# Kernel optimization log

Hardware: AMD Instinct MI355X
Metric: run time of the kernel (lower is better)

## Reference

```python
import jax, jax.numpy as jnp
import numpy as np


def bilinear_resize(x, out_h, out_w):
    # x: [B, C, H, W]; matches torch F.interpolate(mode='bilinear', align_corners=False)
    B, C, H, W = x.shape
    ry = jnp.clip((jnp.arange(out_h, dtype=jnp.float32) + 0.5) * (H / out_h) - 0.5, 0.0, H - 1)
    rx = jnp.clip((jnp.arange(out_w, dtype=jnp.float32) + 0.5) * (W / out_w) - 0.5, 0.0, W - 1)
    y0 = jnp.floor(ry).astype(jnp.int32); y1 = jnp.minimum(y0 + 1, H - 1)
    x0 = jnp.floor(rx).astype(jnp.int32); x1 = jnp.minimum(x0 + 1, W - 1)
    wy = (ry - y0)[:, None]  # [out_h,1]
    wx = (rx - x0)[None, :]  # [1,out_w]
    r0 = x[:, :, y0, :]; r1 = x[:, :, y1, :]
    v00 = r0[:, :, :, x0]; v01 = r0[:, :, :, x1]
    v10 = r1[:, :, :, x0]; v11 = r1[:, :, :, x1]
    return (v00 * (1 - wx) + v01 * wx) * (1 - wy) + (v10 * (1 - wx) + v11 * wx) * wy


def setup_inputs() -> dict:
    key0 = jax.random.key(0)
    ks = jax.random.split(key0, 16)
    B, N, C, H = 2, 300, 256, 8
    hw_lvl = np.array([[64, 64], [32, 32], [16, 16]], dtype=np.int64)
    L = int((hw_lvl[:, 0] * hw_lvl[:, 1]).sum())  # 5376
    p = lambda k, sh: (0.02 * jax.random.normal(k, sh, dtype=jnp.float32))
    return {
        'query': jax.random.normal(ks[0], (B, N, C), dtype=jnp.float32),
        'key': jax.random.normal(ks[1], (B, L, C), dtype=jnp.float32),
        'value': jax.random.normal(ks[2], (B, L, C), dtype=jnp.float32),
        'key_padding_mask': jnp.zeros((B, L), dtype=bool),
        'hw_lvl': hw_lvl,
        'Wq': p(ks[3], (C, C)), 'Wk': p(ks[4], (C, C)), 'Wv': p(ks[5], (C, C)),
        'Wp': p(ks[6], (C, C)), 'bp': jnp.zeros((C,), jnp.float32),
        'W1': p(ks[7], (H, H)), 'b1': jnp.zeros((H,), jnp.float32),
        'W2': p(ks[8], (H, H)), 'b2': jnp.zeros((H,), jnp.float32),
        'W3': p(ks[9], (H, H)), 'b3': jnp.zeros((H,), jnp.float32),
        'Wm': p(ks[10], (3 * H, 1)), 'bm': jnp.zeros((1,), jnp.float32),
    }


def reference(query, key, value, key_padding_mask, hw_lvl,
              Wq, Wk, Wv, Wp, bp, W1, b1, W2, b2, W3, b3, Wm, bm):
    hw = np.asarray(hw_lvl)
    h1, wd1 = int(hw[0, 0]), int(hw[0, 1])
    h2, wd2 = int(hw[1, 0]), int(hw[1, 1])
    h3, wd3 = int(hw[2, 0]), int(hw[2, 1])
    w1 = h1 * wd1
    w2 = w1 + h2 * wd2
    B, N, C = query.shape
    L = key.shape[1]
    H = W1.shape[0]
    scale = (C // H) ** -0.5

    q = (query @ Wq).reshape(B, N, H, C // H)
    k = (key @ Wk).reshape(B, L, H, C // H)
    v = (value @ Wv).reshape(B, L, H, C // H)
    attn = jnp.einsum('bnhd,blhd->bhnl', q, k) * scale  # [B,H,N,L]

    ap = attn.transpose(0, 2, 3, 1)  # [B,N,L,H]
    f1 = jax.nn.relu(ap[:, :, :w1] @ W1 + b1)                      # [B,N,w1,H]
    f2 = jax.nn.relu(ap[:, :, w1:w2] @ W2 + b2)                    # [B,N,h2*wd2,H]
    f3 = jax.nn.relu(ap[:, :, w2:] @ W3 + b3)                      # [B,N,h3*wd3,H]
    f2 = f2.transpose(0, 1, 3, 2).reshape(B * N, H, h2, wd2)
    f3 = f3.transpose(0, 1, 3, 2).reshape(B * N, H, h3, wd3)
    f2 = bilinear_resize(f2, h1, wd1).transpose(0, 2, 3, 1).reshape(B, N, w1, H)
    f3 = bilinear_resize(f3, h1, wd1).transpose(0, 2, 3, 1).reshape(B, N, w1, H)
    new_feats = jnp.concatenate([f1, f2, f3], axis=-1)             # [B,N,w1,3H]
    mask = jax.nn.relu(new_feats @ Wm + bm)                        # [B,N,w1,1]

    aw = jax.nn.softmax(attn, axis=-1)                             # [B,H,N,L]
    x = jnp.einsum('bhnl,blhd->bnhd', aw, v).reshape(B, N, C)
    x = x @ Wp + bp
    return x, mask
```

## Files before the change

kernel.cpp:

```cpp
#include <hip/hip_runtime.h>
#include <hip/hip_bf16.h>

typedef __hip_bfloat16 bf16;
typedef __attribute__((ext_vector_type(8))) short short8v;
typedef __attribute__((ext_vector_type(8))) unsigned short ushort8v;
typedef __attribute__((ext_vector_type(4))) unsigned short ushort4v;
typedef __attribute__((ext_vector_type(4))) float float4v;

__device__ __forceinline__ float bfu2f(unsigned short u) {
    union { unsigned int i; float f; } v; v.i = ((unsigned int)u) << 16; return v.f;
}
__device__ __forceinline__ unsigned short f2bfu_rn(float x) {
    union { float f; unsigned int i; } u; u.f = x;
    unsigned int r = (u.i + 0x7FFFu + ((u.i >> 16) & 1u)) >> 16;
    return (unsigned short)r;
}

__global__ __launch_bounds__(256) void cast_wt(
    const float* __restrict__ Wq, const float* __restrict__ Wk,
    const float* __restrict__ Wv, const float* __restrict__ Wp,
    unsigned short* __restrict__ wt)
{
    __shared__ unsigned short tile[64][72];
    const float* W = (blockIdx.z == 0) ? Wq : (blockIdx.z == 1) ? Wk
                   : (blockIdx.z == 2) ? Wv : Wp;
    unsigned short* WT = wt + (size_t)blockIdx.z * 65536;
    const int t = threadIdx.x;
    const int k0 = blockIdx.x * 64, n0 = blockIdx.y * 64;
    {
        const int r = t >> 2, cseg = (t & 3) * 16;
        const float* src = W + (size_t)(k0 + r) * 256 + n0 + cseg;
        #pragma unroll
        for (int j = 0; j < 16; ++j) tile[r][cseg + j] = f2bfu_rn(src[j]);
    }
    __syncthreads();
    {
        const int ch = t & 63, lq = t >> 6;
        ushort8v o0, o1;
        #pragma unroll
        for (int i = 0; i < 8; ++i) o0[i] = tile[lq * 16 + i][ch];
        #pragma unroll
        for (int i = 0; i < 8; ++i) o1[i] = tile[lq * 16 + 8 + i][ch];
        unsigned short* dst = WT + (size_t)(n0 + ch) * 256 + k0 + lq * 16;
        *(ushort8v*)(dst)     = o0;
        *(ushort8v*)(dst + 8) = o1;
    }
}

__device__ __forceinline__ void proj_core(
    const float* __restrict__ aptr, const unsigned short* __restrict__ Wt,
    int nc0, int m16, int quad, float4v acc[8])
{
    #pragma unroll
    for (int i = 0; i < 8; ++i) acc[i] = (float4v){0.f, 0.f, 0.f, 0.f};
    #pragma unroll
    for (int ks = 0; ks < 8; ++ks) {
        float4 a0 = *(const float4*)(aptr + ks * 32);
        float4 a1 = *(const float4*)(aptr + ks * 32 + 4);
        short8v af;
        af[0] = (short)f2bfu_rn(a0.x); af[1] = (short)f2bfu_rn(a0.y);
        af[2] = (short)f2bfu_rn(a0.z); af[3] = (short)f2bfu_rn(a0.w);
        af[4] = (short)f2bfu_rn(a1.x); af[5] = (short)f2bfu_rn(a1.y);
        af[6] = (short)f2bfu_rn(a1.z); af[7] = (short)f2bfu_rn(a1.w);
        #pragma unroll
        for (int i = 0; i < 8; ++i) {
            short8v bfr = *(const short8v*)(Wt + (size_t)(nc0 + i * 16 + m16) * 256 + ks * 32 + quad * 8);
            acc[i] = __builtin_amdgcn_mfma_f32_16x16x32_bf16(af, bfr, acc[i], 0, 0, 0);
        }
    }
}

__global__ __launch_bounds__(256) void proj_all(
    const float* __restrict__ q, const float* __restrict__ k, const float* __restrict__ v,
    const unsigned short* __restrict__ wt,
    unsigned short* __restrict__ qb, unsigned short* __restrict__ kb,
    unsigned short* __restrict__ vt)
{
    const int t = threadIdx.x;
    const int wave = t >> 6, lane = t & 63;
    const int m16 = lane & 15, quad = lane >> 4;
    const int msub = (wave & 1) * 16;
    const int nc0 = (wave >> 1) * 128;
    const int bx = blockIdx.x;

    float4v acc[8];
    if (bx < 19) {
        const int m0 = bx * 32;
        const int arow = min(m0 + msub + m16, 599);
        proj_core(q + (size_t)arow * 256 + quad * 8, wt, nc0, m16, quad, acc);
        #pragma unroll
        for (int i = 0; i < 8; ++i)
            #pragma unroll
            for (int r = 0; r < 4; ++r) {
                int m = m0 + msub + quad * 4 + r;
                if (m < 600)
                    qb[(size_t)m * 256 + nc0 + i * 16 + m16] = f2bfu_rn(acc[i][r]);
            }
    } else if (bx < 355) {
        const int m0 = (bx - 19) * 32;
        proj_core(k + (size_t)(m0 + msub + m16) * 256 + quad * 8, wt + 65536, nc0, m16, quad, acc);
        #pragma unroll
        for (int i = 0; i < 8; ++i)
            #pragma unroll
            for (int r = 0; r < 4; ++r) {
                int m = m0 + msub + quad * 4 + r;
                kb[(size_t)m * 256 + nc0 + i * 16 + m16] = f2bfu_rn(acc[i][r]);
            }
    } else {
        const int m0 = (bx - 355) * 32;
        proj_core(v + (size_t)(m0 + msub + m16) * 256 + quad * 8, wt + 131072, nc0, m16, quad, acc);
        const int bb = (m0 >= 5376) ? 1 : 0;
        const int lcol = m0 - bb * 5376 + msub + quad * 4;
        #pragma unroll
        for (int i = 0; i < 8; ++i) {
            const int ch = nc0 + i * 16 + m16;
            ushort4v p;
            #pragma unroll
            for (int r = 0; r < 4; ++r) p[r] = f2bfu_rn(acc[i][r]);
            *(ushort4v*)(vt + (size_t)(bb * 256 + ch) * 5376 + lcol) = p;
        }
    }
}

__global__ __launch_bounds__(512) void attn_fused(
    const unsigned short* __restrict__ qb, const unsigned short* __restrict__ kb,
    const unsigned short* __restrict__ vt,
    const float* __restrict__ W1, const float* __restrict__ b1,
    const float* __restrict__ W2, const float* __restrict__ b2,
    const float* __restrict__ W3, const float* __restrict__ b3,
    const float* __restrict__ Wm,
    float* __restrict__ xbp, float* __restrict__ Sp,
    float* __restrict__ g2, float* __restrict__ g3, float* __restrict__ maskp)
{
    __shared__ unsigned short probs[8][16 * 136];
    __shared__ float wT[64];
    __shared__ float blv[8], wmv[8];

    const int t = threadIdx.x;
    const int wave = t >> 6, lane = t & 63;

    const int i0 = blockIdx.x;
    const int m = (i0 & 7) * 200 + (i0 >> 3);
    if (m >= 1596) return;
    const int grp = m / 19, nt = m - grp * 19;
    const int b = grp / 42, zz = grp - b * 42;
    const int n0 = nt * 16;
    const int l0 = zz * 128;
    const int lvl = (zz >= 32) + (zz >= 40);

    const float* Wl = (lvl == 0) ? W1 : (lvl == 1) ? W2 : W3;
    const float* bl = (lvl == 0) ? b1 : (lvl == 1) ? b2 : b3;
    if (t < 64) wT[t] = Wl[(t & 7) * 8 + (t >> 3)];
    if (t < 8)  { blv[t] = bl[t]; wmv[t] = Wm[lvl * 8 + t]; }

    const int m16 = lane & 15, quad = lane >> 4;
    const int h = wave;
    const float scale = 0.17677669529663687f;

    const short8v qfrag = *(const short8v*)(qb + (size_t)(b * 300 + min(n0 + m16, 299)) * 256 + h * 32 + quad * 8);
    const unsigned short* kbase = kb + (size_t)(b * 5376 + l0) * 256 + h * 32 + quad * 8;
    const unsigned short* vt0 = vt + (size_t)(b * 256 + h * 32 + m16) * 5376 + l0;
    const unsigned short* vt1 = vt0 + (size_t)16 * 5376;
    unsigned short* const pw = &probs[wave][0];

    #pragma unroll
    for (int i = 0; i < 8; ++i) {
        short8v kf = *(const short8v*)(kbase + (size_t)(i * 16 + m16) * 256);
        float4v c = {0.f, 0.f, 0.f, 0.f};
        c = __builtin_amdgcn_mfma_f32_16x16x32_bf16(kf, qfrag, c, 0, 0, 0);
        ushort4v pk;
        #pragma unroll
        for (int r = 0; r < 4; ++r) pk[r] = f2bfu_rn(c[r] * scale);
        *(ushort4v*)(pw + m16 * 136 + i * 16 + quad * 4) = pk;
    }
    __syncthreads();

    {
        const int nl = t >> 5;
        const int n = n0 + nl;
        if (n < 300) {
            const int lb = (t & 31) * 4;
            ushort4v u[8];
            #pragma unroll
            for (int hp = 0; hp < 8; ++hp)
                u[hp] = *(const ushort4v*)(&probs[hp][nl * 136 + lb]);
            float4 o;
            float* op = (float*)&o;
            #pragma unroll
            for (int half = 0; half < 2; ++half) {
                float sv[2][8];
                #pragma unroll
                for (int pp = 0; pp < 2; ++pp)
                    #pragma unroll
                    for (int hp = 0; hp < 8; ++hp) sv[pp][hp] = bfu2f(u[hp][half * 2 + pp]);
                float f0 = 0.f, f1 = 0.f;
                #pragma unroll
                for (int hh = 0; hh < 8; ++hh) {
                    const float4 wA = *(const float4*)(&wT[hh * 8]);
                    const float4 wB = *(const float4*)(&wT[hh * 8 + 4]);
                    const float bb_ = blv[hh], wm_ = wmv[hh];
                    float a0 = bb_
                        + sv[0][0] * wA.x + sv[0][1] * wA.y + sv[0][2] * wA.z + sv[0][3] * wA.w
                        + sv[0][4] * wB.x + sv[0][5] * wB.y + sv[0][6] * wB.z + sv[0][7] * wB.w;
                    float a1 = bb_
                        + sv[1][0] * wA.x + sv[1][1] * wA.y + sv[1][2] * wA.z + sv[1][3] * wA.w
                        + sv[1][4] * wB.x + sv[1][5] * wB.y + sv[1][6] * wB.z + sv[1][7] * wB.w;
                    f0 += fmaxf(a0, 0.f) * wm_;
                    f1 += fmaxf(a1, 0.f) * wm_;
                }
                op[half * 2]     = f0;
                op[half * 2 + 1] = f1;
            }
            const size_t bn = (size_t)(b * 300 + n);
            const int p = l0 + lb;
            float* dst = (lvl == 0) ? maskp + bn * 4096 + p
                       : (lvl == 1) ? g2 + bn * 1024 + (p - 4096)
                       :              g3 + bn * 256  + (p - 5120);
            *(float4*)dst = o;
        }
    }

    float4v c0 = {0.f, 0.f, 0.f, 0.f};
    float4v c1 = {0.f, 0.f, 0.f, 0.f};
    float sm = 0.f;
    #pragma unroll
    for (int step = 0; step < 4; ++step) {
        const int lloc = step * 32 + quad * 8;
        ushort8v ua = *(const ushort8v*)(pw + m16 * 136 + lloc);
        short8v af;
        #pragma unroll
        for (int j = 0; j < 8; ++j) {
            float e = __expf(bfu2f(ua[j]));
            sm += e;
            af[j] = (short)f2bfu_rn(e);
        }
        short8v bb0 = *(const short8v*)(vt0 + lloc);
        short8v bb1 = *(const short8v*)(vt1 + lloc);
        c0 = __builtin_amdgcn_mfma_f32_16x16x32_bf16(af, bb0, c0, 0, 0, 0);
        c1 = __builtin_amdgcn_mfma_f32_16x16x32_bf16(af, bb1, c1, 0, 0, 0);
    }

    sm += __shfl_xor(sm, 16);
    sm += __shfl_xor(sm, 32);
    float* xplane = xbp + (size_t)zz * 153600;
    float* splane = Sp + (size_t)zz * 4800;
    if (lane < 16 && n0 + lane < 300)
        splane[(size_t)(b * 300 + n0 + lane) * 8 + h] = sm;
    #pragma unroll
    for (int r = 0; r < 4; ++r) {
        const int n = n0 + quad * 4 + r;
        if (n < 300) {
            float* o = xplane + (size_t)(b * 300 + n) * 256 + h * 32 + m16;
            o[0]  = c0[r];
            o[16] = c1[r];
        }
    }
}

__global__ __launch_bounds__(256) void finish(
    const float* __restrict__ g2, const float* __restrict__ g3,
    const float* __restrict__ xbp, const float* __restrict__ Sp,
    float* __restrict__ xr, float* __restrict__ Sr,
    const float* __restrict__ bmp, float* __restrict__ out)
{
    const int t = threadIdx.x;
    if (blockIdx.x < 600) {
        __shared__ float gs[1280];
        __shared__ float bms;
        const int bn = blockIdx.x;
        if (t == 0) bms = bmp[0];
        ((float4v*)gs)[t] = ((const float4v*)(g2 + (size_t)bn * 1024))[t];
        if (t < 64) ((float4v*)(gs + 1024))[t] = ((const float4v*)(g3 + (size_t)bn * 256))[t];
        __syncthreads();

        float* mp = out + 153600 + (size_t)bn * 4096;
        #pragma unroll
        for (int it = 0; it < 4; ++it) {
            const int p0 = it * 1024 + t * 4;
            float4v mv = *(const float4v*)(mp + p0);
            float4v res;
            #pragma unroll
            for (int pp = 0; pp < 4; ++pp) {
                const int p = p0 + pp;
                const int Y = p >> 6, X = p & 63;
                float acc = mv[pp] + bms;
                {
                    float ry = fminf(fmaxf(0.5f * Y - 0.25f, 0.f), 31.f);
                    float rx = fminf(fmaxf(0.5f * X - 0.25f, 0.f), 31.f);
                    int y0 = (int)ry, x0 = (int)rx;
                    int y1 = min(y0 + 1, 31), x1 = min(x0 + 1, 31);
                    float wy = ry - (float)y0, wx = rx - (float)x0;
                    acc += (gs[y0 * 32 + x0] * (1.f - wx) + gs[y0 * 32 + x1] * wx) * (1.f - wy)
                         + (gs[y1 * 32 + x0] * (1.f - wx) + gs[y1 * 32 + x1] * wx) * wy;
                }
                {
                    float ry = fminf(fmaxf(0.25f * Y - 0.375f, 0.f), 15.f);
                    float rx = fminf(fmaxf(0.25f * X - 0.375f, 0.f), 15.f);
                    int y0 = (int)ry, x0 = (int)rx;
                    int y1 = min(y0 + 1, 15), x1 = min(x0 + 1, 15);
                    float wy = ry - (float)y0, wx = rx - (float)x0;
                    acc += (gs[1024 + y0 * 16 + x0] * (1.f - wx) + gs[1024 + y0 * 16 + x1] * wx) * (1.f - wy)
                         + (gs[1024 + y1 * 16 + x0] * (1.f - wx) + gs[1024 + y1 * 16 + x1] * wx) * wy;
                }
                res[pp] = fmaxf(acc, 0.f);
            }
            *(float4v*)(mp + p0) = res;
        }
    } else {
        const int idx = (blockIdx.x - 600) * 256 + t;
        if (idx < 38400) {
            float4v s = {0.f, 0.f, 0.f, 0.f};
            #pragma unroll 7
            for (int z = 0; z < 42; ++z)
                s += *(const float4v*)(xbp + (size_t)z * 153600 + (size_t)idx * 4);
            *(float4v*)(xr + (size_t)idx * 4) = s;
        } else if (idx < 38400 + 1200) {
            const int si = (idx - 38400) * 4;
            float4v s = {0.f, 0.f, 0.f, 0.f};
            #pragma unroll 7
            for (int z = 0; z < 42; ++z)
                s += *(const float4v*)(Sp + (size_t)z * 4800 + si);
            *(float4v*)(Sr + si) = s;
        }
    }
}

__global__ __launch_bounds__(256) void proj_out(
    const float* __restrict__ xr, const float* __restrict__ Sr,
    const unsigned short* __restrict__ Wtp,
    const float* __restrict__ bpv, float* __restrict__ out)
{
    const int t = threadIdx.x;
    const int wave = t >> 6, lane = t & 63;
    const int m16 = lane & 15, quad = lane >> 4;
    const int nc0 = wave * 64;
    const int m0 = blockIdx.x * 16;
    const int arow = min(m0 + m16, 599);
    const float* a0p = xr + (size_t)arow * 256 + quad * 8;

    float4v acc[4];
    #pragma unroll
    for (int i = 0; i < 4; ++i) acc[i] = (float4v){0.f, 0.f, 0.f, 0.f};

    #pragma unroll
    for (int ks = 0; ks < 8; ++ks) {
        const float rS = 1.0f / Sr[(size_t)arow * 8 + ks];
        float4 x0 = *(const float4*)(a0p + ks * 32);
        float4 x1 = *(const float4*)(a0p + ks * 32 + 4);
        short8v af;
        af[0] = (short)f2bfu_rn(x0.x * rS); af[1] = (short)f2bfu_rn(x0.y * rS);
        af[2] = (short)f2bfu_rn(x0.z * rS); af[3] = (short)f2bfu_rn(x0.w * rS);
        af[4] = (short)f2bfu_rn(x1.x * rS); af[5] = (short)f2bfu_rn(x1.y * rS);
        af[6] = (short)f2bfu_rn(x1.z * rS); af[7] = (short)f2bfu_rn(x1.w * rS);
        #pragma unroll
        for (int i = 0; i < 4; ++i) {
            short8v bfr = *(const short8v*)(Wtp + (size_t)(nc0 + i * 16 + m16) * 256 + ks * 32 + quad * 8);
            acc[i] = __builtin_amdgcn_mfma_f32_16x16x32_bf16(af, bfr, acc[i], 0, 0, 0);
        }
    }

    #pragma unroll
    for (int i = 0; i < 4; ++i) {
        const float bv = bpv[nc0 + i * 16 + m16];
        #pragma unroll
        for (int r = 0; r < 4; ++r) {
            int mm = m0 + quad * 4 + r;
            if (mm < 600)
                out[(size_t)mm * 256 + nc0 + i * 16 + m16] = acc[i][r] + bv;
        }
    }
}

extern "C" void kernel_launch(void* const* d_in, const int* in_sizes, int n_in,
                              void* d_out, int out_size, void* d_ws, size_t ws_size,
                              hipStream_t stream) {
    const float* query = (const float*)d_in[0];
    const float* key   = (const float*)d_in[1];
    const float* value = (const float*)d_in[2];
    const float* Wq = (const float*)d_in[5];
    const float* Wk = (const float*)d_in[6];
    const float* Wv = (const float*)d_in[7];
    const float* Wp = (const float*)d_in[8];
    const float* bp = (const float*)d_in[9];
    const float* W1 = (const float*)d_in[10];
    const float* b1 = (const float*)d_in[11];
    const float* W2 = (const float*)d_in[12];
    const float* b2 = (const float*)d_in[13];
    const float* W3 = (const float*)d_in[14];
    const float* b3 = (const float*)d_in[15];
    const float* Wm = (const float*)d_in[16];
    const float* bm = (const float*)d_in[17];
    float* out = (float*)d_out;

    char* ws = (char*)d_ws;
    unsigned short* wt = (unsigned short*)(ws);
    bf16*  qb   = (bf16*) (ws + 524288);
    bf16*  kb   = (bf16*) (ws + 831488);
    bf16*  vt   = (bf16*) (ws + 6336512);
    float* xbp  = (float*)(ws + 11841536);
    float* Sp   = (float*)(ws + 37646336);
    float* g2   = (float*)(ws + 38452736);
    float* g3   = (float*)(ws + 40910336);
    float* xr   = (float*)(ws + 41524736);
    float* Sr   = (float*)(ws + 42139136);
    float* maskp = out + 153600;

    cast_wt<<<dim3(4, 4, 4), 256, 0, stream>>>(Wq, Wk, Wv, Wp, wt);

    proj_all<<<691, 256, 0, stream>>>(query, key, value, wt,
        (unsigned short*)qb, (unsigned short*)kb, (unsigned short*)vt);

    attn_fused<<<1600, 512, 0, stream>>>(
        (const unsigned short*)qb, (const unsigned short*)kb, (const unsigned short*)vt,
        W1, b1, W2, b2, W3, b3, Wm, xbp, Sp, g2, g3, maskp);

    finish<<<755, 256, 0, stream>>>(g2, g3, xbp, Sp, xr, Sr, bm, out);

    proj_out<<<38, 256, 0, stream>>>(xr, Sr, (const unsigned short*)wt + 196608, bp, out);
}
```

Before: 191.6 us.

## Store K and V projections in head-major tiled layouts for contiguous attention loads

The K projection output is written as [batch][head][L][32] instead of row-major [L][256], and V-transpose is written in a blocked [batch][head][L/8][32][8] layout. The attention kernel's K fragment loads and V MFMA operand loads then read contiguous memory per wave instead of striding by 256 or 5376 elements. The projection-side stores become more scattered, with 2-byte K stores at a stride of 32 elements, in exchange for better-coalesced reads in the attention kernel.

Result: faster. 183.7 us (-4.1%).

```diff
diff --git a/kernel.cpp b/kernel.cpp
--- a/kernel.cpp
+++ b/kernel.cpp
@@ -99,25 +99,33 @@
     } else if (bx < 355) {
         const int m0 = (bx - 19) * 32;
         proj_core(k + (size_t)(m0 + msub + m16) * 256 + quad * 8, wt + 65536, nc0, m16, quad, acc);
-        #pragma unroll
-        for (int i = 0; i < 8; ++i)
-            #pragma unroll
-            for (int r = 0; r < 4; ++r) {
-                int m = m0 + msub + quad * 4 + r;
-                kb[(size_t)m * 256 + nc0 + i * 16 + m16] = f2bfu_rn(acc[i][r]);
-            }
+        const int bb = (m0 >= 5376) ? 1 : 0;
+        const int lb0 = m0 - bb * 5376 + msub + quad * 4;
+        const int hbase = (wave >> 1) * 4;
+        #pragma unroll
+        for (int i = 0; i < 8; ++i) {
+            const int hh = hbase + (i >> 1);
+            const int c16 = (i & 1) * 16;
+            unsigned short* kdst = kb + ((size_t)(bb * 8 + hh) * 5376 + lb0) * 32 + c16 + m16;
+            #pragma unroll
+            for (int r = 0; r < 4; ++r)
+                kdst[(size_t)r * 32] = f2bfu_rn(acc[i][r]);
+        }
     } else {
         const int m0 = (bx - 355) * 32;
         proj_core(v + (size_t)(m0 + msub + m16) * 256 + quad * 8, wt + 131072, nc0, m16, quad, acc);
         const int bb = (m0 >= 5376) ? 1 : 0;
-        const int lcol = m0 - bb * 5376 + msub + quad * 4;
+        const int lb0 = m0 - bb * 5376 + msub + quad * 4;
+        const int g0 = lb0 >> 3, e0 = lb0 & 7;
+        const int hbase = (wave >> 1) * 4;
         #pragma unroll
         for (int i = 0; i < 8; ++i) {
-            const int ch = nc0 + i * 16 + m16;
+            const int hh = hbase + (i >> 1);
+            const int cc = (i & 1) * 16 + m16;
             ushort4v p;
             #pragma unroll
             for (int r = 0; r < 4; ++r) p[r] = f2bfu_rn(acc[i][r]);
-            *(ushort4v*)(vt + (size_t)(bb * 256 + ch) * 5376 + lcol) = p;
+            *(ushort4v*)(vt + (((size_t)(bb * 8 + hh) * 672 + g0) * 32 + cc) * 8 + e0) = p;
         }
     }
 }
@@ -158,14 +166,13 @@
     const float scale = 0.17677669529663687f;
 
     const short8v qfrag = *(const short8v*)(qb + (size_t)(b * 300 + min(n0 + m16, 299)) * 256 + h * 32 + quad * 8);
-    const unsigned short* kbase = kb + (size_t)(b * 5376 + l0) * 256 + h * 32 + quad * 8;
-    const unsigned short* vt0 = vt + (size_t)(b * 256 + h * 32 + m16) * 5376 + l0;
-    const unsigned short* vt1 = vt0 + (size_t)16 * 5376;
+    const unsigned short* kbase = kb + ((size_t)(b * 8 + h) * 5376 + l0) * 32 + quad * 8;
+    const unsigned short* vtb = vt + ((size_t)(b * 8 + h) * 672 + (l0 >> 3)) * 256 + quad * 256 + m16 * 8;
     unsigned short* const pw = &probs[wave][0];
 
     #pragma unroll
     for (int i = 0; i < 8; ++i) {
-        short8v kf = *(const short8v*)(kbase + (size_t)(i * 16 + m16) * 256);
+        short8v kf = *(const short8v*)(kbase + (size_t)(i * 16 + m16) * 32);
         float4v c = {0.f, 0.f, 0.f, 0.f};
         c = __builtin_amdgcn_mfma_f32_16x16x32_bf16(kf, qfrag, c, 0, 0, 0);
         ushort4v pk;
@@ -234,8 +241,8 @@
             sm += e;
             af[j] = (short)f2bfu_rn(e);
         }
-        short8v bb0 = *(const short8v*)(vt0 + lloc);
-        short8v bb1 = *(const short8v*)(vt1 + lloc);
+        short8v bb0 = *(const short8v*)(vtb + step * 1024);
+        short8v bb1 = *(const short8v*)(vtb + step * 1024 + 128);
         c0 = __builtin_amdgcn_mfma_f32_16x16x32_bf16(af, bb0, c0, 0, 0, 0);
         c1 = __builtin_amdgcn_mfma_f32_16x16x32_bf16(af, bb1, c1, 0, 0, 0);
     }
```
